# Optimization experiments

Measured on AMD Instinct MI355X. Metric: run time of the kernel, lower is better.

Reference implementation:

```python
import jax, jax.numpy as jnp
import numpy as np

D_MODEL = 1024
NUM_HEADS = 16
HEAD_DIM = D_MODEL // NUM_HEADS


def setup_inputs() -> dict:
    key = jax.random.key(0)
    ks = jax.random.split(key, 5)
    s = 1.0 / np.sqrt(D_MODEL)
    return {
        "x": jax.random.normal(ks[0], (4, 2048, D_MODEL), dtype=jnp.float32),
        "w_qkv": jax.random.uniform(ks[1], (3 * D_MODEL, D_MODEL), jnp.float32, -s, s),
        "b_qkv": jax.random.uniform(ks[2], (3 * D_MODEL,), jnp.float32, -s, s),
        "w_out": jax.random.uniform(ks[3], (D_MODEL, D_MODEL), jnp.float32, -s, s),
        "b_out": jax.random.uniform(ks[4], (D_MODEL,), jnp.float32, -s, s),
    }


def reference(x, w_qkv, b_qkv, w_out, b_out):
    B, T, D = x.shape
    # torch Linear: y = x @ W^T + b
    qkv = x @ w_qkv.T + b_qkv                                  # [B,T,3D]
    qkv = qkv.reshape(B, T, 3, NUM_HEADS, HEAD_DIM)
    q, k, v = jnp.moveaxis(qkv, 2, 0)                          # each [B,T,H,Hd]
    q = q.transpose(0, 2, 1, 3)                                # [B,H,T,Hd]
    k = k.transpose(0, 2, 1, 3)
    v = v.transpose(0, 2, 1, 3)
    scale = 1.0 / np.sqrt(HEAD_DIM).astype(np.float32)
    scores = jnp.einsum("bhqd,bhkd->bhqk", q, k) * scale       # [B,H,T,T]
    attn = jax.nn.softmax(scores, axis=-1)
    out = jnp.einsum("bhqk,bhkd->bhqd", attn, v)               # [B,H,T,Hd]
    out = out.transpose(0, 2, 1, 3).reshape(B, T, D)
    return out @ w_out.T + b_out
```

## Files before the change

### kernel.cpp

```cpp
#include <hip/hip_runtime.h>
#include <hip/hip_bf16.h>

#define SEQLEN  2048
#define DMODEL  1024
#define NHEADS  16
#define BT_ROWS 8192

typedef __attribute__((ext_vector_type(8))) _Float16 half8;
typedef __attribute__((ext_vector_type(4))) _Float16 half4;
typedef __attribute__((ext_vector_type(2))) _Float16 half2v;
typedef __attribute__((ext_vector_type(4))) float f32x4;
typedef unsigned short u16;

#define MFMAH(A, B, C)  __builtin_amdgcn_mfma_f32_16x16x32_f16((A), (B), (C), 0, 0, 0)

static __device__ __forceinline__ float fast_exp2(float x) {
#if __has_builtin(__builtin_amdgcn_exp2f)
    return __builtin_amdgcn_exp2f(x);
#else
    return exp2f(x);
#endif
}

typedef const __attribute__((address_space(1))) unsigned int* gas_t;
typedef __attribute__((address_space(3))) unsigned int* las_t;
static __device__ __forceinline__ void gld16(const void* g, void* l) {
    __builtin_amdgcn_global_load_lds((gas_t)g, (las_t)l, 16, 0, 0);
}

static __device__ __forceinline__ unsigned pack_f16x2(float a, float b) {
    return __builtin_bit_cast(unsigned, __builtin_amdgcn_cvt_pkrtz(a, b));
}

__global__ __launch_bounds__(256)
void cvt_f16(const float* __restrict__ in, u16* __restrict__ outp, int n4)
{
    int i = blockIdx.x * 256 + threadIdx.x;
    const int stride = gridDim.x * 256;
    for (; i < n4; i += stride) {
        const float4 v = ((const float4*)in)[i];
        const float f[4] = {v.x, v.y, v.z, v.w};
        ushort4 h4;
        u16 hh[4];
#pragma unroll
        for (int j = 0; j < 4; ++j)
            hh[j] = __builtin_bit_cast(u16, (_Float16)f[j]);
        h4.x = hh[0]; h4.y = hh[1]; h4.z = hh[2]; h4.w = hh[3];
        *(ushort4*)(outp + (size_t)i * 4) = h4;
    }
}

template<int MODE>
__global__ __launch_bounds__(256)
void gemm_nt_mfma(const u16* __restrict__ Af, const u16* __restrict__ Bf,
                  const float* __restrict__ bias, float* __restrict__ Cf,
                  u16* __restrict__ Pq, u16* __restrict__ Pk,
                  u16* __restrict__ Pv)
{
    __shared__ _Float16 Ah[128 * 32];
    __shared__ _Float16 Bh[128 * 32];

    const int tid  = threadIdx.x;
    const int lane = tid & 63;
    const int w    = tid >> 6;
    const int l15  = lane & 15;
    const int lg   = lane >> 4;
    const int wm   = w & 1;
    const int wn   = w >> 1;
    const int rowBase = blockIdx.y * 128;
    const int colBase = blockIdx.x * 128;

    const int srow = lane >> 2;
    const int sc   = lane & 3;

    f32x4 acc[4][4];
#pragma unroll
    for (int m = 0; m < 4; ++m)
#pragma unroll
        for (int n = 0; n < 4; ++n) acc[m][n] = (f32x4){0.f, 0.f, 0.f, 0.f};

    auto stage = [&](int kt) {
        const int k0 = kt * 32;
#pragma unroll
        for (int i = 0; i < 2; ++i) {
            const int slab = w * 2 + i;
            const int row  = slab * 16 + srow;
            const int gc   = sc ^ ((row >> 1) & 3);
            const size_t aoff = (size_t)(rowBase + row) * 1024 + k0 + gc * 8;
            const size_t boff = (size_t)(colBase + row) * 1024 + k0 + gc * 8;
            gld16(Af + aoff, &Ah[slab * 512]);
            gld16(Bf + boff, &Bh[slab * 512]);
        }
    };

    stage(0);

    for (int kt = 0; kt < 32; ++kt) {
        __syncthreads();

        half8 afh[4], bfh[4];
#pragma unroll
        for (int m = 0; m < 4; ++m) {
            const int row = wm * 64 + m * 16 + l15;
            const int cR  = lg ^ ((row >> 1) & 3);
            afh[m] = *(const half8*)&Ah[row * 32 + cR * 8];
        }
#pragma unroll
        for (int n = 0; n < 4; ++n) {
            const int row = wn * 64 + n * 16 + l15;
            const int cR  = lg ^ ((row >> 1) & 3);
            bfh[n] = *(const half8*)&Bh[row * 32 + cR * 8];
        }

        __syncthreads();
        if (kt < 31) stage(kt + 1);

        __builtin_amdgcn_s_setprio(1);
#pragma unroll
        for (int m = 0; m < 4; ++m)
#pragma unroll
            for (int n = 0; n < 4; ++n)
                acc[m][n] = MFMAH(afh[m], bfh[n], acc[m][n]);
        __builtin_amdgcn_s_setprio(0);
    }

    float bv[4];
#pragma unroll
    for (int n = 0; n < 4; ++n)
        bv[n] = bias[colBase + wn * 64 + n * 16 + l15];

    if constexpr (MODE == 0) {
#pragma unroll
        for (int m = 0; m < 4; ++m)
#pragma unroll
            for (int n = 0; n < 4; ++n) {
                const int col = colBase + wn * 64 + n * 16 + l15;
#pragma unroll
                for (int r = 0; r < 4; ++r) {
                    const int row = rowBase + wm * 64 + m * 16 + lg * 4 + r;
                    Cf[(size_t)row * 1024 + col] = acc[m][n][r] + bv[n];
                }
            }
    } else {
        const int comp = colBase >> 10;
        const float scale = (comp == 0) ? (0.125f * 1.44269504f) : 1.0f;
        u16* hp = (comp == 0) ? Pq : ((comp == 1) ? Pk : Pv);
        const int colc0 = colBase & 1023;
#pragma unroll
        for (int m = 0; m < 4; ++m)
#pragma unroll
            for (int n = 0; n < 4; ++n) {
                const int col = colc0 + wn * 64 + n * 16 + l15;
#pragma unroll
                for (int r = 0; r < 4; ++r) {
                    const int row = rowBase + wm * 64 + m * 16 + lg * 4 + r;
                    const float v = (acc[m][n][r] + bv[n]) * scale;
                    hp[(size_t)row * 1024 + col] =
                        __builtin_bit_cast(u16, (_Float16)v);
                }
            }
    }
}

__global__ __launch_bounds__(256, 2)
void flash_attn_mfma(const u16* __restrict__ Qf, const u16* __restrict__ Kf,
                     const u16* __restrict__ Vf, u16* __restrict__ Of)
{
    __shared__ __align__(16) _Float16 Kh[64 * 64];
    __shared__ __align__(16) _Float16 Vt[64][72];
    __shared__ __align__(16) _Float16 Pl[4][64][72];

    const int tid  = threadIdx.x;
    const int lane = tid & 63;
    const int w    = tid >> 6;
    const int l15  = lane & 15;
    const int lg   = lane >> 4;

    const int raw = blockIdx.x;
    const int swz = (raw & 7) * 64 + (raw >> 3);
    const int bh  = swz >> 3;
    const int qb  = swz & 7;
    const int b   = bh >> 4;
    const int h   = bh & 15;

    const int qRow0 = b * SEQLEN + qb * 256 + w * 64;
    const int kRowB = b * SEQLEN;
    const int hc    = h * 64;

    half8 Qr[4][2];
#pragma unroll
    for (int qt = 0; qt < 4; ++qt)
#pragma unroll
        for (int g = 0; g < 2; ++g) {
            const size_t off = (size_t)(qRow0 + qt * 16 + l15) * 1024
                             + hc + g * 32 + lg * 8;
            Qr[qt][g] = *(const half8*)(Qf + off);
        }

    f32x4 O[4][4];
    f32x4 accL[4];
#pragma unroll
    for (int qt = 0; qt < 4; ++qt) {
        accL[qt] = (f32x4){0.f, 0.f, 0.f, 0.f};
#pragma unroll
        for (int dt = 0; dt < 4; ++dt) O[qt][dt] = (f32x4){0.f, 0.f, 0.f, 0.f};
    }
    half8 vones;
#pragma unroll
    for (int j = 0; j < 8; ++j) vones[j] = (_Float16)1.0f;

    const int vp  = tid & 31;
    const int kv0 = (vp & 15) | ((vp >> 4) << 5);
    const int pcol = (kv0 & 15) * 4 + (kv0 >> 4);
    const int d0  = (tid >> 5) * 8;

    half8 kreg[2], vreg0, vreg1;
    int krow[2], kcc[2];

    auto load_tile = [&](int kt) {
#pragma unroll
        for (int i = 0; i < 2; ++i) {
            const int s = tid + 256 * i;
            const int row = s >> 3;
            const int c   = s & 7;
            krow[i] = row; kcc[i] = c;
            const int gc = c ^ (row & 7);
            const size_t g = (size_t)(kRowB + kt * 64 + row) * 1024 + hc + gc * 8;
            kreg[i] = *(const half8*)(Kf + g);
        }
        const size_t g = (size_t)(kRowB + kt * 64 + kv0) * 1024 + hc + d0;
        vreg0 = *(const half8*)(Vf + g);
        vreg1 = *(const half8*)(Vf + g + (size_t)16 * 1024);
    };

    load_tile(0);

    for (int kt = 0; kt < SEQLEN / 64; ++kt) {
        __syncthreads();
#pragma unroll
        for (int i = 0; i < 2; ++i)
            *(half8*)&Kh[krow[i] * 64 + kcc[i] * 8] = kreg[i];
#pragma unroll
        for (int j = 0; j < 8; ++j) {
            half2v pv;
            pv[0] = vreg0[j]; pv[1] = vreg1[j];
            *(half2v*)&Vt[d0 + j][pcol] = pv;
        }
        __syncthreads();

        if (kt < SEQLEN / 64 - 1) load_tile(kt + 1);

        half8 kf[4][2];
#pragma unroll
        for (int k4 = 0; k4 < 4; ++k4) {
            const int row = k4 * 16 + l15;
            const int swk = row & 7;
            kf[k4][0] = *(const half8*)&Kh[row * 64 + ((lg     ^ swk) * 8)];
            kf[k4][1] = *(const half8*)&Kh[row * 64 + (((4+lg) ^ swk) * 8)];
        }

#pragma unroll
        for (int qt = 0; qt < 4; ++qt) {
            f32x4 S[4];
#pragma unroll
            for (int k4 = 0; k4 < 4; ++k4) S[k4] = (f32x4){0.f, 0.f, 0.f, 0.f};

            __builtin_amdgcn_s_setprio(1);
#pragma unroll
            for (int k4 = 0; k4 < 4; ++k4) {
                S[k4] = MFMAH(Qr[qt][0], kf[k4][0], S[k4]);
                S[k4] = MFMAH(Qr[qt][1], kf[k4][1], S[k4]);
            }
            __builtin_amdgcn_s_setprio(0);

#pragma unroll
            for (int r = 0; r < 4; ++r) {
                const float p0 = fast_exp2(S[0][r]);
                const float p1 = fast_exp2(S[1][r]);
                const float p2 = fast_exp2(S[2][r]);
                const float p3 = fast_exp2(S[3][r]);
                uint2 pw;
                pw.x = pack_f16x2(p0, p1);
                pw.y = pack_f16x2(p2, p3);
                *(uint2*)&Pl[w][qt * 16 + lg * 4 + r][l15 * 4] = pw;
            }
        }

        asm volatile("s_waitcnt lgkmcnt(0)" ::: "memory");
        __builtin_amdgcn_sched_barrier(0);

        __builtin_amdgcn_s_setprio(1);
#pragma unroll
        for (int ks = 0; ks < 2; ++ks) {
            half8 Pf[4];
#pragma unroll
            for (int qt = 0; qt < 4; ++qt)
                Pf[qt] = *(const half8*)&Pl[w][qt * 16 + l15][ks * 32 + lg * 8];
#pragma unroll
            for (int dt = 0; dt < 4; ++dt) {
                const half8 Vfr = *(const half8*)&Vt[dt * 16 + l15][ks * 32 + lg * 8];
#pragma unroll
                for (int qt = 0; qt < 4; ++qt)
                    O[qt][dt] = MFMAH(Pf[qt], Vfr, O[qt][dt]);
            }
#pragma unroll
            for (int qt = 0; qt < 4; ++qt)
                accL[qt] = MFMAH(Pf[qt], vones, accL[qt]);
        }
        __builtin_amdgcn_s_setprio(0);
    }

#pragma unroll
    for (int qt = 0; qt < 4; ++qt)
#pragma unroll
        for (int r = 0; r < 4; ++r) {
            const float inv = 1.0f / accL[qt][r];
            const int row = qRow0 + qt * 16 + lg * 4 + r;
#pragma unroll
            for (int dt = 0; dt < 4; ++dt) {
                const float o = O[qt][dt][r] * inv;
                const size_t off = (size_t)row * 1024 + hc + dt * 16 + l15;
                Of[off] = __builtin_bit_cast(u16, (_Float16)o);
            }
        }
}

extern "C" void kernel_launch(void* const* d_in, const int* in_sizes, int n_in,
                              void* d_out, int out_size, void* d_ws, size_t ws_size,
                              hipStream_t stream)
{
    const float* x     = (const float*)d_in[0];
    const float* w_qkv = (const float*)d_in[1];
    const float* b_qkv = (const float*)d_in[2];
    const float* w_out = (const float*)d_in[3];
    const float* b_out = (const float*)d_in[4];
    float* out = (float*)d_out;

    const size_t PLANE = (size_t)BT_ROWS * DMODEL;
    u16* Qf  = (u16*)d_ws;
    u16* Kf  = Qf + PLANE;
    u16* Vf  = Kf + PLANE;
    u16* xF  = Vf + PLANE;
    u16* aF  = xF;
    u16* wqkvF = xF + PLANE;
    u16* woutF = wqkvF + (size_t)3072 * 1024;

    cvt_f16<<<2048, 256, 0, stream>>>(x, xF, (int)(PLANE / 4));
    cvt_f16<<<768, 256, 0, stream>>>(w_qkv, wqkvF, 3072 * 1024 / 4);
    cvt_f16<<<256, 256, 0, stream>>>(w_out, woutF, 1024 * 1024 / 4);

    gemm_nt_mfma<1><<<dim3(3072 / 128, BT_ROWS / 128), 256, 0, stream>>>(
        xF, wqkvF, b_qkv, nullptr, Qf, Kf, Vf);

    flash_attn_mfma<<<dim3(512), 256, 0, stream>>>(Qf, Kf, Vf, aF);

    gemm_nt_mfma<0><<<dim3(DMODEL / 128, BT_ROWS / 128), 256, 0, stream>>>(
        aF, woutF, b_out, out, nullptr, nullptr, nullptr);
}
```

Measured before the change: 196.4 us.

## Switch attention to 32x32 MFMA with register-resident P via permlane swap

Rewrites the flash attention inner loop to use 32x32x16 MFMA tiles and compute S transposed (K as A operand). The exponentiated probabilities stay in registers, rearranged with permlane32 swaps into the operand layout for the PV MFMA, so the per-wave P round-trip through LDS and its wait are removed. K tiles are now double-buffered and loaded directly into LDS with global_load_lds, and V uses an XOR-swizzled transpose layout. This adds lane-permute work and changes the register footprint, which could affect occupancy.

Result: slower. 204.1 us (+3.9%).

```diff
diff --git a/kernel.cpp b/kernel.cpp
--- a/kernel.cpp
+++ b/kernel.cpp
@@ -6,13 +6,14 @@
 #define NHEADS  16
 #define BT_ROWS 8192
 
-typedef __attribute__((ext_vector_type(8))) _Float16 half8;
-typedef __attribute__((ext_vector_type(4))) _Float16 half4;
-typedef __attribute__((ext_vector_type(2))) _Float16 half2v;
-typedef __attribute__((ext_vector_type(4))) float f32x4;
+typedef __attribute__((ext_vector_type(8)))  _Float16 half8;
+typedef __attribute__((ext_vector_type(2)))  _Float16 half2v;
+typedef __attribute__((ext_vector_type(4)))  float    f32x4;
+typedef __attribute__((ext_vector_type(16))) float    f32x16;
 typedef unsigned short u16;
 
 #define MFMAH(A, B, C)  __builtin_amdgcn_mfma_f32_16x16x32_f16((A), (B), (C), 0, 0, 0)
+#define MFMA32(A, B, C) __builtin_amdgcn_mfma_f32_32x32x16_f16((A), (B), (C), 0, 0, 0)
 
 static __device__ __forceinline__ float fast_exp2(float x) {
 #if __has_builtin(__builtin_amdgcn_exp2f)
@@ -30,6 +31,20 @@
 
 static __device__ __forceinline__ unsigned pack_f16x2(float a, float b) {
     return __builtin_bit_cast(unsigned, __builtin_amdgcn_cvt_pkrtz(a, b));
+}
+
+static __device__ __forceinline__ void plane_swap(unsigned &a, unsigned &b) {
+#if __has_builtin(__builtin_amdgcn_permlane32_swap)
+    auto r = __builtin_amdgcn_permlane32_swap(a, b, false, false);
+    a = r[0]; b = r[1];
+#else
+    const int lane = (int)(threadIdx.x & 63);
+    const unsigned ax = __shfl(a, lane ^ 32);
+    const unsigned bx = __shfl(b, lane ^ 32);
+    const unsigned na = (lane & 32) ? bx : a;
+    const unsigned nb = (lane & 32) ? b : ax;
+    a = na; b = nb;
+#endif
 }
 
 __global__ __launch_bounds__(256)
@@ -166,15 +181,14 @@
 void flash_attn_mfma(const u16* __restrict__ Qf, const u16* __restrict__ Kf,
                      const u16* __restrict__ Vf, u16* __restrict__ Of)
 {
-    __shared__ __align__(16) _Float16 Kh[64 * 64];
-    __shared__ __align__(16) _Float16 Vt[64][72];
-    __shared__ __align__(16) _Float16 Pl[4][64][72];
+    __shared__ __align__(16) _Float16 Kh[2][64 * 64];
+    __shared__ __align__(16) _Float16 Vt[64 * 64];
 
     const int tid  = threadIdx.x;
     const int lane = tid & 63;
+    const int l31  = lane & 31;
+    const int hi   = lane >> 5;
     const int w    = tid >> 6;
-    const int l15  = lane & 15;
-    const int lg   = lane >> 4;
 
     const int raw = blockIdx.x;
     const int swz = (raw & 7) * 64 + (raw >> 3);
@@ -187,140 +201,140 @@
     const int kRowB = b * SEQLEN;
     const int hc    = h * 64;
 
-    half8 Qr[4][2];
-#pragma unroll
-    for (int qt = 0; qt < 4; ++qt)
-#pragma unroll
-        for (int g = 0; g < 2; ++g) {
-            const size_t off = (size_t)(qRow0 + qt * 16 + l15) * 1024
-                             + hc + g * 32 + lg * 8;
-            Qr[qt][g] = *(const half8*)(Qf + off);
-        }
-
-    f32x4 O[4][4];
-    f32x4 accL[4];
-#pragma unroll
-    for (int qt = 0; qt < 4; ++qt) {
-        accL[qt] = (f32x4){0.f, 0.f, 0.f, 0.f};
-#pragma unroll
-        for (int dt = 0; dt < 4; ++dt) O[qt][dt] = (f32x4){0.f, 0.f, 0.f, 0.f};
+    half8 Qr[2][4];
+#pragma unroll
+    for (int qt = 0; qt < 2; ++qt)
+#pragma unroll
+        for (int ds = 0; ds < 4; ++ds) {
+            const size_t off = (size_t)(qRow0 + qt * 32 + l31) * 1024
+                             + hc + ds * 16 + hi * 8;
+            Qr[qt][ds] = *(const half8*)(Qf + off);
+        }
+
+    f32x16 O[2][2];
+    f32x16 accL[2];
+#pragma unroll
+    for (int qt = 0; qt < 2; ++qt) {
+#pragma unroll
+        for (int r = 0; r < 16; ++r) accL[qt][r] = 0.f;
+#pragma unroll
+        for (int dt = 0; dt < 2; ++dt)
+#pragma unroll
+            for (int r = 0; r < 16; ++r) O[qt][dt][r] = 0.f;
     }
     half8 vones;
 #pragma unroll
     for (int j = 0; j < 8; ++j) vones[j] = (_Float16)1.0f;
 
-    const int vp  = tid & 31;
-    const int kv0 = (vp & 15) | ((vp >> 4) << 5);
-    const int pcol = (kv0 & 15) * 4 + (kv0 >> 4);
-    const int d0  = (tid >> 5) * 8;
-
-    half8 kreg[2], vreg0, vreg1;
-    int krow[2], kcc[2];
-
-    auto load_tile = [&](int kt) {
+    const int kv0 = (tid & 31) * 2;
+    const int vd0 = (tid >> 5) * 8;
+    half8 vreg0, vreg1;
+
+    auto stageK = [&](int kt, int buf) {
 #pragma unroll
         for (int i = 0; i < 2; ++i) {
-            const int s = tid + 256 * i;
+            const int s   = tid + 256 * i;
             const int row = s >> 3;
-            const int c   = s & 7;
-            krow[i] = row; kcc[i] = c;
-            const int gc = c ^ (row & 7);
-            const size_t g = (size_t)(kRowB + kt * 64 + row) * 1024 + hc + gc * 8;
-            kreg[i] = *(const half8*)(Kf + g);
-        }
-        const size_t g = (size_t)(kRowB + kt * 64 + kv0) * 1024 + hc + d0;
+            const int cl  = s & 7;
+            const int gc  = cl ^ (row & 7);
+            gld16(Kf + (size_t)(kRowB + kt * 64 + row) * 1024 + hc + gc * 8,
+                  &Kh[buf][row * 64 + cl * 8]);
+        }
+    };
+    auto loadV = [&](int kt) {
+        const size_t g = (size_t)(kRowB + kt * 64 + kv0) * 1024 + hc + vd0;
         vreg0 = *(const half8*)(Vf + g);
-        vreg1 = *(const half8*)(Vf + g + (size_t)16 * 1024);
+        vreg1 = *(const half8*)(Vf + g + 1024);
     };
 
-    load_tile(0);
+    stageK(0, 0);
+    loadV(0);
 
     for (int kt = 0; kt < SEQLEN / 64; ++kt) {
+        const int cur = kt & 1;
         __syncthreads();
 #pragma unroll
-        for (int i = 0; i < 2; ++i)
-            *(half8*)&Kh[krow[i] * 64 + kcc[i] * 8] = kreg[i];
-#pragma unroll
         for (int j = 0; j < 8; ++j) {
+            const int d = vd0 + j;
+            const int c = (kv0 >> 3) ^ (d & 7);
             half2v pv;
             pv[0] = vreg0[j]; pv[1] = vreg1[j];
-            *(half2v*)&Vt[d0 + j][pcol] = pv;
+            *(half2v*)&Vt[d * 64 + c * 8 + (kv0 & 7)] = pv;
         }
         __syncthreads();
-
-        if (kt < SEQLEN / 64 - 1) load_tile(kt + 1);
-
-        half8 kf[4][2];
-#pragma unroll
-        for (int k4 = 0; k4 < 4; ++k4) {
-            const int row = k4 * 16 + l15;
-            const int swk = row & 7;
-            kf[k4][0] = *(const half8*)&Kh[row * 64 + ((lg     ^ swk) * 8)];
-            kf[k4][1] = *(const half8*)&Kh[row * 64 + (((4+lg) ^ swk) * 8)];
-        }
-
-#pragma unroll
-        for (int qt = 0; qt < 4; ++qt) {
-            f32x4 S[4];
-#pragma unroll
-            for (int k4 = 0; k4 < 4; ++k4) S[k4] = (f32x4){0.f, 0.f, 0.f, 0.f};
+        if (kt < SEQLEN / 64 - 1) {
+            stageK(kt + 1, cur ^ 1);
+            loadV(kt + 1);
+        }
+
+#pragma unroll
+        for (int kv32 = 0; kv32 < 2; ++kv32) {
+            half8 kfr[4];
+#pragma unroll
+            for (int ds = 0; ds < 4; ++ds) {
+                const int kv = kv32 * 32 + l31;
+                const int c  = (ds * 2 + hi) ^ (kv & 7);
+                kfr[ds] = *(const half8*)&Kh[cur][kv * 64 + c * 8];
+            }
+
+            half8 Pa[2][2];
+#pragma unroll
+            for (int qt = 0; qt < 2; ++qt) {
+                f32x16 S;
+#pragma unroll
+                for (int r = 0; r < 16; ++r) S[r] = 0.f;
+                __builtin_amdgcn_s_setprio(1);
+#pragma unroll
+                for (int ds = 0; ds < 4; ++ds)
+                    S = MFMA32(kfr[ds], Qr[qt][ds], S);
+                __builtin_amdgcn_s_setprio(0);
+
+                unsigned pk[8];
+#pragma unroll
+                for (int t = 0; t < 8; ++t) {
+                    const float pa = fast_exp2(S[2 * t]);
+                    const float pb = fast_exp2(S[2 * t + 1]);
+                    pk[t] = pack_f16x2(pa, pb);
+                }
+#pragma unroll
+                for (int ks = 0; ks < 2; ++ks) {
+                    unsigned s0 = pk[4 * ks + 0], s2 = pk[4 * ks + 2];
+                    unsigned s1 = pk[4 * ks + 1], s3 = pk[4 * ks + 3];
+                    plane_swap(s0, s2);
+                    plane_swap(s1, s3);
+                    uint4 u; u.x = s0; u.y = s1; u.z = s2; u.w = s3;
+                    Pa[qt][ks] = __builtin_bit_cast(half8, u);
+                }
+                accL[qt] = MFMA32(Pa[qt][0], vones, accL[qt]);
+                accL[qt] = MFMA32(Pa[qt][1], vones, accL[qt]);
+            }
 
             __builtin_amdgcn_s_setprio(1);
 #pragma unroll
-            for (int k4 = 0; k4 < 4; ++k4) {
-                S[k4] = MFMAH(Qr[qt][0], kf[k4][0], S[k4]);
-                S[k4] = MFMAH(Qr[qt][1], kf[k4][1], S[k4]);
-            }
+            for (int ks = 0; ks < 2; ++ks)
+#pragma unroll
+                for (int dt = 0; dt < 2; ++dt) {
+                    const int d = dt * 32 + l31;
+                    const int c = (kv32 * 4 + ks * 2 + hi) ^ (d & 7);
+                    const half8 Vfr = *(const half8*)&Vt[d * 64 + c * 8];
+                    O[0][dt] = MFMA32(Pa[0][ks], Vfr, O[0][dt]);
+                    O[1][dt] = MFMA32(Pa[1][ks], Vfr, O[1][dt]);
+                }
             __builtin_amdgcn_s_setprio(0);
-
-#pragma unroll
-            for (int r = 0; r < 4; ++r) {
-                const float p0 = fast_exp2(S[0][r]);
-                const float p1 = fast_exp2(S[1][r]);
-                const float p2 = fast_exp2(S[2][r]);
-                const float p3 = fast_exp2(S[3][r]);
-                uint2 pw;
-                pw.x = pack_f16x2(p0, p1);
-                pw.y = pack_f16x2(p2, p3);
-                *(uint2*)&Pl[w][qt * 16 + lg * 4 + r][l15 * 4] = pw;
-            }
-        }
-
-        asm volatile("s_waitcnt lgkmcnt(0)" ::: "memory");
-        __builtin_amdgcn_sched_barrier(0);
-
-        __builtin_amdgcn_s_setprio(1);
-#pragma unroll
-        for (int ks = 0; ks < 2; ++ks) {
-            half8 Pf[4];
-#pragma unroll
-            for (int qt = 0; qt < 4; ++qt)
-                Pf[qt] = *(const half8*)&Pl[w][qt * 16 + l15][ks * 32 + lg * 8];
-#pragma unroll
-            for (int dt = 0; dt < 4; ++dt) {
-                const half8 Vfr = *(const half8*)&Vt[dt * 16 + l15][ks * 32 + lg * 8];
-#pragma unroll
-                for (int qt = 0; qt < 4; ++qt)
-                    O[qt][dt] = MFMAH(Pf[qt], Vfr, O[qt][dt]);
-            }
-#pragma unroll
-            for (int qt = 0; qt < 4; ++qt)
-                accL[qt] = MFMAH(Pf[qt], vones, accL[qt]);
-        }
-        __builtin_amdgcn_s_setprio(0);
-    }
-
-#pragma unroll
-    for (int qt = 0; qt < 4; ++qt)
-#pragma unroll
-        for (int r = 0; r < 4; ++r) {
+        }
+    }
+
+#pragma unroll
+    for (int qt = 0; qt < 2; ++qt)
+#pragma unroll
+        for (int r = 0; r < 16; ++r) {
             const float inv = 1.0f / accL[qt][r];
-            const int row = qRow0 + qt * 16 + lg * 4 + r;
-#pragma unroll
-            for (int dt = 0; dt < 4; ++dt) {
+            const int q = qRow0 + qt * 32 + (r & 3) + 8 * (r >> 2) + 4 * hi;
+#pragma unroll
+            for (int dt = 0; dt < 2; ++dt) {
                 const float o = O[qt][dt][r] * inv;
-                const size_t off = (size_t)row * 1024 + hc + dt * 16 + l15;
-                Of[off] = __builtin_bit_cast(u16, (_Float16)o);
+                Of[(size_t)q * 1024 + hc + dt * 32 + l31] =
+                    __builtin_bit_cast(u16, (_Float16)o);
             }
         }
 }
```
